# Kernel optimization log

Measured on AMD Instinct MI355X. Metric: run time of the kernel, lower is better.

Reference implementation:

```python
import jax, jax.numpy as jnp
import numpy as np


def setup_inputs() -> dict:
    key = jax.random.key(0)
    ks = jax.random.split(key, 12)
    B, N, M, C = 2, 20000, 4096, 6
    S, K, J = 2, 25, 64          # scales, grid cells (2*2+1)^2, neighbors per cell
    Cin = C + 2                   # xy coords concatenated to features
    Cout = 64
    xyz = jax.random.normal(ks[0], (B, N, 3), dtype=jnp.float32)
    feature = jax.random.normal(ks[1], (B, N, C), dtype=jnp.float32)
    new_xyz = jax.random.normal(ks[2], (B, M, 3), dtype=jnp.float32)
    idx = jax.random.randint(ks[3], (S, B, M, K, J), 0, N, dtype=jnp.int32)
    weight = jax.random.uniform(ks[4], (S, B, M, K, J), dtype=jnp.float32)
    conv_w = jax.random.normal(ks[5], (Cout, Cin, K), dtype=jnp.float32) * 0.05
    conv_b = jnp.zeros((Cout,), dtype=jnp.float32)
    mlp_w0 = jax.random.normal(ks[6], (128, S * Cout), dtype=jnp.float32) * 0.05
    mlp_b0 = jnp.zeros((128,), dtype=jnp.float32)
    mlp_w1 = jax.random.normal(ks[7], (256, 128), dtype=jnp.float32) * 0.05
    mlp_b1 = jnp.zeros((256,), dtype=jnp.float32)
    return {"xyz": xyz, "feature": feature, "new_xyz": new_xyz, "idx": idx,
            "weight": weight, "conv_w": conv_w, "conv_b": conv_b,
            "mlp_w0": mlp_w0, "mlp_b0": mlp_b0, "mlp_w1": mlp_w1, "mlp_b1": mlp_b1}


def reference(xyz, feature, new_xyz, idx, weight, conv_w, conv_b,
              mlp_w0, mlp_b0, mlp_w1, mlp_b1):
    # xyz_feature = cat(xy, feature): (B, N, Cin)
    xf = jnp.concatenate([xyz[:, :, :2], feature], axis=-1)
    center2 = new_xyz[:, :, :2]  # (B, M, 2); remaining channels of center are zero

    def per_scale(idx_s, w_s):
        # idx_s, w_s: (B, M, K, J). Gather neighbor features then bilinear-weight.
        gathered = jax.vmap(lambda f, i: f[i])(xf, idx_s)     # (B, M, K, J, Cin)
        nf = jnp.einsum('bmkj,bmkjc->bmkc', w_s, gathered)    # (B, M, K, Cin)
        nf = nf.at[..., :2].add(-center2[:, :, None, :])      # subtract center (xy only)
        # conv2d with kernel (1, K) over the neighbor axis + ReLU
        out = jnp.einsum('bmkc,ock->bom', nf, conv_w) + conv_b[None, :, None]
        return jax.nn.relu(out)                                # (B, Cout, M)

    outs = [per_scale(idx[s], weight[s]) for s in range(idx.shape[0])]
    x = jnp.concatenate(outs, axis=1)                          # (B, S*Cout, M)
    # SharedMLP: 1x1 convs with ReLU (bn=False)
    x = jax.nn.relu(jnp.einsum('bcm,oc->bom', x, mlp_w0) + mlp_b0[None, :, None])
    x = jax.nn.relu(jnp.einsum('bcm,oc->bom', x, mlp_w1) + mlp_b1[None, :, None])
    result_feature = jnp.transpose(x, (0, 2, 1))               # (B, M, 256)
    return new_xyz, result_feature
```

## Files before the change

### kernel.cpp

```cpp
#include <hip/hip_runtime.h>

#define B 2
#define N 20000
#define M 4096
#define S 2
#define K 25
#define J 64
#define CIN 8
#define KJ (K*J)
#define TC 32
#define XP 36

__global__ __launch_bounds__(256) void prep_kernel(
    const float* __restrict__ xyz, const float* __restrict__ feature,
    const float* __restrict__ new_xyz, const float* __restrict__ conv_w,
    const float* __restrict__ w0, const float* __restrict__ w1,
    float* __restrict__ xf, float* __restrict__ conv_wT,
    float* __restrict__ w0T, float* __restrict__ w1T,
    float* __restrict__ out_newxyz) {
    const int T1 = B * N * CIN;
    const int T2 = 208 * 64;
    const int T3 = B * M * 3;
    const int T4 = 128 * 128;
    const int T5 = 128 * 256;
    int e = blockIdx.x * blockDim.x + threadIdx.x;
    if (e < T1) {
        int r = e >> 3, t = e & 7;
        xf[e] = (t < 2) ? xyz[r * 3 + t] : feature[r * 6 + (t - 2)];
    } else if (e < T1 + T2) {
        int e2 = e - T1;
        int i = e2 >> 6, o = e2 & 63;
        conv_wT[e2] = (i < 200) ? conv_w[o * 200 + (i & 7) * 25 + (i >> 3)] : 0.f;
    } else if (e < T1 + T2 + T3) {
        int e3 = e - T1 - T2;
        out_newxyz[e3] = new_xyz[e3];
    } else if (e < T1 + T2 + T3 + T4) {
        int e4 = e - T1 - T2 - T3;
        int c = e4 >> 7, o = e4 & 127;
        w0T[e4] = w0[o * 128 + c];
    } else if (e < T1 + T2 + T3 + T4 + T5) {
        int e5 = e - T1 - T2 - T3 - T4;
        int c = e5 >> 8, o = e5 & 255;
        w1T[e5] = w1[o * 128 + c];
    }
}

__global__ __launch_bounds__(256) void gather_conv_kernel(
    const int* __restrict__ idx, const float* __restrict__ weight,
    const float* __restrict__ new_xyz, const float* __restrict__ xf,
    const float* __restrict__ conv_wT, const float* __restrict__ conv_b,
    float* __restrict__ xmid) {
    __shared__ float snf[208];
    __shared__ float spart[4][64];

    int g = blockIdx.x;
    int m = g & (M - 1);
    int sb = g >> 12;
    int b = sb & (B - 1);
    int s = sb >> 1;
    int tid = threadIdx.x;

    if (tid >= 200 && tid < 208) snf[tid] = 0.f;

    if (tid < 200) {
        int k = tid >> 3, jg = tid & 7;
        (void)k;
        const int4*   gi4 = (const int4*)  (idx    + (size_t)g * KJ);
        const float4* gw4 = (const float4*)(weight + (size_t)g * KJ);
        int4   ia = gi4[tid * 2], ib = gi4[tid * 2 + 1];
        float4 wa = gw4[tid * 2], wb = gw4[tid * 2 + 1];

        const float4* xfb = (const float4*)(xf + (size_t)b * N * CIN);
        float acc[8] = {0.f,0.f,0.f,0.f,0.f,0.f,0.f,0.f};
        int   rows[8] = {ia.x, ia.y, ia.z, ia.w, ib.x, ib.y, ib.z, ib.w};
        float wsv[8]  = {wa.x, wa.y, wa.z, wa.w, wb.x, wb.y, wb.z, wb.w};
        #pragma unroll
        for (int j = 0; j < 8; ++j) {
            float4 lo = xfb[rows[j] * 2];
            float4 hi = xfb[rows[j] * 2 + 1];
            float w = wsv[j];
            acc[0] = fmaf(w, lo.x, acc[0]);
            acc[1] = fmaf(w, lo.y, acc[1]);
            acc[2] = fmaf(w, lo.z, acc[2]);
            acc[3] = fmaf(w, lo.w, acc[3]);
            acc[4] = fmaf(w, hi.x, acc[4]);
            acc[5] = fmaf(w, hi.y, acc[5]);
            acc[6] = fmaf(w, hi.z, acc[6]);
            acc[7] = fmaf(w, hi.w, acc[7]);
        }
        #pragma unroll
        for (int d = 1; d < 8; d <<= 1) {
            #pragma unroll
            for (int c = 0; c < 8; ++c) acc[c] += __shfl_xor(acc[c], d, 64);
        }
        if (jg == 0) {
            int kk = tid >> 3;
            float cx = new_xyz[(b * M + m) * 3 + 0];
            float cy = new_xyz[(b * M + m) * 3 + 1];
            acc[0] -= cx; acc[1] -= cy;
            float4* s4 = (float4*)&snf[kk * 8];
            s4[0] = make_float4(acc[0], acc[1], acc[2], acc[3]);
            s4[1] = make_float4(acc[4], acc[5], acc[6], acc[7]);
        }
    }
    __syncthreads();

    int o = tid & 63, p = tid >> 6;
    const float4* snf4 = (const float4*)snf;
    float acc2 = 0.f;
    #pragma unroll
    for (int q = 0; q < 13; ++q) {
        float4 v = snf4[p * 13 + q];
        int i = (p * 13 + q) * 4;
        acc2 = fmaf(v.x, conv_wT[(i + 0) * 64 + o], acc2);
        acc2 = fmaf(v.y, conv_wT[(i + 1) * 64 + o], acc2);
        acc2 = fmaf(v.z, conv_wT[(i + 2) * 64 + o], acc2);
        acc2 = fmaf(v.w, conv_wT[(i + 3) * 64 + o], acc2);
    }
    spart[p][o] = acc2;
    __syncthreads();

    if (tid < 64) {
        float v = spart[0][tid] + spart[1][tid] + spart[2][tid] + spart[3][tid] + conv_b[tid];
        v = fmaxf(v, 0.f);
        xmid[((size_t)(b * M + m)) * 128 + s * 64 + tid] = v;
    }
}

__global__ __launch_bounds__(256) void mlp_kernel(
    const float* __restrict__ xmid,
    const float* __restrict__ w0T, const float* __restrict__ b0,
    const float* __restrict__ w1T, const float* __restrict__ b1,
    float* __restrict__ out_rf) {
    __shared__ float xs[128 * XP];
    __shared__ float ys0[128 * XP];

    int tid = threadIdx.x;
    int col0 = blockIdx.x * TC;

    {
        const float4* xm4 = (const float4*)(xmid + (size_t)col0 * 128);
        #pragma unroll
        for (int r = tid; r < 32 * TC; r += 256) {
            int lc = r >> 5, c4 = r & 31;
            float4 v = xm4[lc * 32 + c4];
            int c = c4 * 4;
            xs[(c + 0) * XP + lc] = v.x;
            xs[(c + 1) * XP + lc] = v.y;
            xs[(c + 2) * XP + lc] = v.z;
            xs[(c + 3) * XP + lc] = v.w;
        }
    }
    __syncthreads();

    {
        int og = tid >> 3, cg = tid & 7;
        int o0 = og * 4, lc0 = cg * 4;
        float acc[4][4];
        #pragma unroll
        for (int i = 0; i < 4; ++i) {
            float bv = b0[o0 + i];
            #pragma unroll
            for (int u = 0; u < 4; ++u) acc[i][u] = bv;
        }
        for (int c = 0; c < 128; ++c) {
            float4 xv = *(const float4*)&xs[c * XP + lc0];
            float4 wv = *(const float4*)&w0T[c * 128 + o0];
            acc[0][0] = fmaf(wv.x, xv.x, acc[0][0]);
            acc[0][1] = fmaf(wv.x, xv.y, acc[0][1]);
            acc[0][2] = fmaf(wv.x, xv.z, acc[0][2]);
            acc[0][3] = fmaf(wv.x, xv.w, acc[0][3]);
            acc[1][0] = fmaf(wv.y, xv.x, acc[1][0]);
            acc[1][1] = fmaf(wv.y, xv.y, acc[1][1]);
            acc[1][2] = fmaf(wv.y, xv.z, acc[1][2]);
            acc[1][3] = fmaf(wv.y, xv.w, acc[1][3]);
            acc[2][0] = fmaf(wv.z, xv.x, acc[2][0]);
            acc[2][1] = fmaf(wv.z, xv.y, acc[2][1]);
            acc[2][2] = fmaf(wv.z, xv.z, acc[2][2]);
            acc[2][3] = fmaf(wv.z, xv.w, acc[2][3]);
            acc[3][0] = fmaf(wv.w, xv.x, acc[3][0]);
            acc[3][1] = fmaf(wv.w, xv.y, acc[3][1]);
            acc[3][2] = fmaf(wv.w, xv.z, acc[3][2]);
            acc[3][3] = fmaf(wv.w, xv.w, acc[3][3]);
        }
        #pragma unroll
        for (int i = 0; i < 4; ++i)
            #pragma unroll
            for (int u = 0; u < 4; ++u)
                ys0[(o0 + i) * XP + lc0 + u] = fmaxf(acc[i][u], 0.f);
    }
    __syncthreads();

    {
        int og = tid >> 2, cg = tid & 3;
        int o0 = og * 4, lc0 = cg * 8;
        float acc[4][8];
        #pragma unroll
        for (int i = 0; i < 4; ++i) {
            float bv = b1[o0 + i];
            #pragma unroll
            for (int u = 0; u < 8; ++u) acc[i][u] = bv;
        }
        for (int c = 0; c < 128; ++c) {
            float4 xa = *(const float4*)&ys0[c * XP + lc0];
            float4 xb = *(const float4*)&ys0[c * XP + lc0 + 4];
            float4 wv = *(const float4*)&w1T[c * 256 + o0];
            float xv[8] = {xa.x, xa.y, xa.z, xa.w, xb.x, xb.y, xb.z, xb.w};
            #pragma unroll
            for (int i = 0; i < 4; ++i) {
                float w = (i == 0) ? wv.x : (i == 1) ? wv.y : (i == 2) ? wv.z : wv.w;
                #pragma unroll
                for (int u = 0; u < 8; ++u)
                    acc[i][u] = fmaf(w, xv[u], acc[i][u]);
            }
        }
        #pragma unroll
        for (int u = 0; u < 8; ++u) {
            float4 v = make_float4(fmaxf(acc[0][u], 0.f), fmaxf(acc[1][u], 0.f),
                                   fmaxf(acc[2][u], 0.f), fmaxf(acc[3][u], 0.f));
            *(float4*)&out_rf[(size_t)(col0 + lc0 + u) * 256 + o0] = v;
        }
    }
}

extern "C" void kernel_launch(void* const* d_in, const int* in_sizes, int n_in,
                              void* d_out, int out_size, void* d_ws, size_t ws_size,
                              hipStream_t stream) {
    const float* xyz     = (const float*)d_in[0];
    const float* feature = (const float*)d_in[1];
    const float* new_xyz = (const float*)d_in[2];
    const int*   idx     = (const int*)  d_in[3];
    const float* weight  = (const float*)d_in[4];
    const float* conv_w  = (const float*)d_in[5];
    const float* conv_b  = (const float*)d_in[6];
    const float* mlp_w0  = (const float*)d_in[7];
    const float* mlp_b0  = (const float*)d_in[8];
    const float* mlp_w1  = (const float*)d_in[9];
    const float* mlp_b1  = (const float*)d_in[10];

    float* out    = (float*)d_out;
    float* out_rf = out + (size_t)B * M * 3;

    float* xf      = (float*)d_ws;
    float* conv_wT = xf + 320000;
    float* xmid    = conv_wT + 13312;
    float* w0T     = xmid + 1048576;
    float* w1T     = w0T + 16384;

    {
        int total = 320000 + 13312 + 24576 + 16384 + 32768;
        int blocks = (total + 255) / 256;
        prep_kernel<<<blocks, 256, 0, stream>>>(xyz, feature, new_xyz, conv_w,
                                                mlp_w0, mlp_w1,
                                                xf, conv_wT, w0T, w1T, out);
    }
    {
        int blocks = S * B * M;
        gather_conv_kernel<<<blocks, 256, 0, stream>>>(idx, weight, new_xyz, xf,
                                                       conv_wT, conv_b, xmid);
    }
    {
        int blocks = (B * M) / TC;
        mlp_kernel<<<blocks, 256, 0, stream>>>(xmid, w0T, mlp_b0, w1T, mlp_b1,
                                               out_rf);
    }
}
```

Baseline: 387.3 us.

## Store gathered point features in bf16 and split MLP into two LDS-weighted kernels

```diff
diff --git a/kernel.cpp b/kernel.cpp
--- a/kernel.cpp
+++ b/kernel.cpp
@@ -1,4 +1,5 @@
 #include <hip/hip_runtime.h>
+#include <hip/hip_bf16.h>
 
 #define B 2
 #define N 20000
@@ -6,19 +7,20 @@
 #define S 2
 #define K 25
 #define J 64
-#define CIN 8
 #define KJ (K*J)
 #define TC 32
 #define XP 36
+
+typedef unsigned int u32;
 
 __global__ __launch_bounds__(256) void prep_kernel(
     const float* __restrict__ xyz, const float* __restrict__ feature,
     const float* __restrict__ new_xyz, const float* __restrict__ conv_w,
     const float* __restrict__ w0, const float* __restrict__ w1,
-    float* __restrict__ xf, float* __restrict__ conv_wT,
+    __hip_bfloat16* __restrict__ xfh, float* __restrict__ conv_wT,
     float* __restrict__ w0T, float* __restrict__ w1T,
     float* __restrict__ out_newxyz) {
-    const int T1 = B * N * CIN;
+    const int T1 = B * N * 8;
     const int T2 = 208 * 64;
     const int T3 = B * M * 3;
     const int T4 = 128 * 128;
@@ -26,7 +28,8 @@
     int e = blockIdx.x * blockDim.x + threadIdx.x;
     if (e < T1) {
         int r = e >> 3, t = e & 7;
-        xf[e] = (t < 2) ? xyz[r * 3 + t] : feature[r * 6 + (t - 2)];
+        float v = (t < 2) ? xyz[r * 3 + t] : feature[r * 6 + (t - 2)];
+        xfh[e] = __float2bfloat16(v);
     } else if (e < T1 + T2) {
         int e2 = e - T1;
         int i = e2 >> 6, o = e2 & 63;
@@ -47,7 +50,7 @@
 
 __global__ __launch_bounds__(256) void gather_conv_kernel(
     const int* __restrict__ idx, const float* __restrict__ weight,
-    const float* __restrict__ new_xyz, const float* __restrict__ xf,
+    const float* __restrict__ new_xyz, const uint4* __restrict__ xfh,
     const float* __restrict__ conv_wT, const float* __restrict__ conv_b,
     float* __restrict__ xmid) {
     __shared__ float snf[208];
@@ -63,37 +66,34 @@
     if (tid >= 200 && tid < 208) snf[tid] = 0.f;
 
     if (tid < 200) {
-        int k = tid >> 3, jg = tid & 7;
-        (void)k;
         const int4*   gi4 = (const int4*)  (idx    + (size_t)g * KJ);
         const float4* gw4 = (const float4*)(weight + (size_t)g * KJ);
         int4   ia = gi4[tid * 2], ib = gi4[tid * 2 + 1];
         float4 wa = gw4[tid * 2], wb = gw4[tid * 2 + 1];
 
-        const float4* xfb = (const float4*)(xf + (size_t)b * N * CIN);
+        const uint4* xfb = xfh + (size_t)b * N;
         float acc[8] = {0.f,0.f,0.f,0.f,0.f,0.f,0.f,0.f};
         int   rows[8] = {ia.x, ia.y, ia.z, ia.w, ib.x, ib.y, ib.z, ib.w};
         float wsv[8]  = {wa.x, wa.y, wa.z, wa.w, wb.x, wb.y, wb.z, wb.w};
         #pragma unroll
         for (int j = 0; j < 8; ++j) {
-            float4 lo = xfb[rows[j] * 2];
-            float4 hi = xfb[rows[j] * 2 + 1];
+            uint4 r = xfb[rows[j]];
             float w = wsv[j];
-            acc[0] = fmaf(w, lo.x, acc[0]);
-            acc[1] = fmaf(w, lo.y, acc[1]);
-            acc[2] = fmaf(w, lo.z, acc[2]);
-            acc[3] = fmaf(w, lo.w, acc[3]);
-            acc[4] = fmaf(w, hi.x, acc[4]);
-            acc[5] = fmaf(w, hi.y, acc[5]);
-            acc[6] = fmaf(w, hi.z, acc[6]);
-            acc[7] = fmaf(w, hi.w, acc[7]);
+            acc[0] = fmaf(w, __uint_as_float(r.x << 16),          acc[0]);
+            acc[1] = fmaf(w, __uint_as_float(r.x & 0xffff0000u),  acc[1]);
+            acc[2] = fmaf(w, __uint_as_float(r.y << 16),          acc[2]);
+            acc[3] = fmaf(w, __uint_as_float(r.y & 0xffff0000u),  acc[3]);
+            acc[4] = fmaf(w, __uint_as_float(r.z << 16),          acc[4]);
+            acc[5] = fmaf(w, __uint_as_float(r.z & 0xffff0000u),  acc[5]);
+            acc[6] = fmaf(w, __uint_as_float(r.w << 16),          acc[6]);
+            acc[7] = fmaf(w, __uint_as_float(r.w & 0xffff0000u),  acc[7]);
         }
         #pragma unroll
         for (int d = 1; d < 8; d <<= 1) {
             #pragma unroll
             for (int c = 0; c < 8; ++c) acc[c] += __shfl_xor(acc[c], d, 64);
         }
-        if (jg == 0) {
+        if ((tid & 7) == 0) {
             int kk = tid >> 3;
             float cx = new_xyz[(b * M + m) * 3 + 0];
             float cy = new_xyz[(b * M + m) * 3 + 1];
@@ -127,17 +127,21 @@
     }
 }
 
-__global__ __launch_bounds__(256) void mlp_kernel(
-    const float* __restrict__ xmid,
-    const float* __restrict__ w0T, const float* __restrict__ b0,
-    const float* __restrict__ w1T, const float* __restrict__ b1,
-    float* __restrict__ out_rf) {
+__global__ __launch_bounds__(256) void mlp0_kernel(
+    float* __restrict__ xmid,
+    const float* __restrict__ w0T, const float* __restrict__ b0) {
+    __shared__ float ws[128 * 128];
     __shared__ float xs[128 * XP];
-    __shared__ float ys0[128 * XP];
 
     int tid = threadIdx.x;
     int col0 = blockIdx.x * TC;
 
+    {
+        const float4* w4 = (const float4*)w0T;
+        float4* ws4 = (float4*)ws;
+        #pragma unroll
+        for (int i = 0; i < 16; ++i) ws4[tid + 256 * i] = w4[tid + 256 * i];
+    }
     {
         const float4* xm4 = (const float4*)(xmid + (size_t)col0 * 128);
         #pragma unroll
@@ -153,73 +157,101 @@
     }
     __syncthreads();
 
-    {
-        int og = tid >> 3, cg = tid & 7;
-        int o0 = og * 4, lc0 = cg * 4;
-        float acc[4][4];
-        #pragma unroll
-        for (int i = 0; i < 4; ++i) {
-            float bv = b0[o0 + i];
-            #pragma unroll
-            for (int u = 0; u < 4; ++u) acc[i][u] = bv;
-        }
-        for (int c = 0; c < 128; ++c) {
-            float4 xv = *(const float4*)&xs[c * XP + lc0];
-            float4 wv = *(const float4*)&w0T[c * 128 + o0];
-            acc[0][0] = fmaf(wv.x, xv.x, acc[0][0]);
-            acc[0][1] = fmaf(wv.x, xv.y, acc[0][1]);
-            acc[0][2] = fmaf(wv.x, xv.z, acc[0][2]);
-            acc[0][3] = fmaf(wv.x, xv.w, acc[0][3]);
-            acc[1][0] = fmaf(wv.y, xv.x, acc[1][0]);
-            acc[1][1] = fmaf(wv.y, xv.y, acc[1][1]);
-            acc[1][2] = fmaf(wv.y, xv.z, acc[1][2]);
-            acc[1][3] = fmaf(wv.y, xv.w, acc[1][3]);
-            acc[2][0] = fmaf(wv.z, xv.x, acc[2][0]);
-            acc[2][1] = fmaf(wv.z, xv.y, acc[2][1]);
-            acc[2][2] = fmaf(wv.z, xv.z, acc[2][2]);
-            acc[2][3] = fmaf(wv.z, xv.w, acc[2][3]);
-            acc[3][0] = fmaf(wv.w, xv.x, acc[3][0]);
-            acc[3][1] = fmaf(wv.w, xv.y, acc[3][1]);
-            acc[3][2] = fmaf(wv.w, xv.z, acc[3][2]);
-            acc[3][3] = fmaf(wv.w, xv.w, acc[3][3]);
-        }
-        #pragma unroll
-        for (int i = 0; i < 4; ++i)
-            #pragma unroll
-            for (int u = 0; u < 4; ++u)
-                ys0[(o0 + i) * XP + lc0 + u] = fmaxf(acc[i][u], 0.f);
+    int og = tid >> 3, cg = tid & 7;
+    int o0 = og * 4, lc0 = cg * 4;
+    float acc[4][4];
+    #pragma unroll
+    for (int i = 0; i < 4; ++i) {
+        float bv = b0[o0 + i];
+        #pragma unroll
+        for (int u = 0; u < 4; ++u) acc[i][u] = bv;
+    }
+    for (int c = 0; c < 128; ++c) {
+        float4 xv = *(const float4*)&xs[c * XP + lc0];
+        float4 wv = *(const float4*)&ws[c * 128 + o0];
+        acc[0][0] = fmaf(wv.x, xv.x, acc[0][0]);
+        acc[0][1] = fmaf(wv.x, xv.y, acc[0][1]);
+        acc[0][2] = fmaf(wv.x, xv.z, acc[0][2]);
+        acc[0][3] = fmaf(wv.x, xv.w, acc[0][3]);
+        acc[1][0] = fmaf(wv.y, xv.x, acc[1][0]);
+        acc[1][1] = fmaf(wv.y, xv.y, acc[1][1]);
+        acc[1][2] = fmaf(wv.y, xv.z, acc[1][2]);
+        acc[1][3] = fmaf(wv.y, xv.w, acc[1][3]);
+        acc[2][0] = fmaf(wv.z, xv.x, acc[2][0]);
+        acc[2][1] = fmaf(wv.z, xv.y, acc[2][1]);
+        acc[2][2] = fmaf(wv.z, xv.z, acc[2][2]);
+        acc[2][3] = fmaf(wv.z, xv.w, acc[2][3]);
+        acc[3][0] = fmaf(wv.w, xv.x, acc[3][0]);
+        acc[3][1] = fmaf(wv.w, xv.y, acc[3][1]);
+        acc[3][2] = fmaf(wv.w, xv.z, acc[3][2]);
+        acc[3][3] = fmaf(wv.w, xv.w, acc[3][3]);
+    }
+    #pragma unroll
+    for (int u = 0; u < 4; ++u) {
+        float4 v = make_float4(fmaxf(acc[0][u], 0.f), fmaxf(acc[1][u], 0.f),
+                               fmaxf(acc[2][u], 0.f), fmaxf(acc[3][u], 0.f));
+        *(float4*)&xmid[(size_t)(col0 + lc0 + u) * 128 + o0] = v;
+    }
+}
+
+__global__ __launch_bounds__(256) void mlp1_kernel(
+    const float* __restrict__ xmid,
+    const float* __restrict__ w1T, const float* __restrict__ b1,
+    float* __restrict__ out_rf) {
+    __shared__ float ws[128 * 256];
+    __shared__ float xs[128 * XP];
+
+    int tid = threadIdx.x;
+    int col0 = blockIdx.x * TC;
+
+    {
+        const float4* w4 = (const float4*)w1T;
+        float4* ws4 = (float4*)ws;
+        #pragma unroll
+        for (int i = 0; i < 32; ++i) ws4[tid + 256 * i] = w4[tid + 256 * i];
+    }
+    {
+        const float4* xm4 = (const float4*)(xmid + (size_t)col0 * 128);
+        #pragma unroll
+        for (int r = tid; r < 32 * TC; r += 256) {
+            int lc = r >> 5, c4 = r & 31;
+            float4 v = xm4[lc * 32 + c4];
+            int c = c4 * 4;
+            xs[(c + 0) * XP + lc] = v.x;
+            xs[(c + 1) * XP + lc] = v.y;
+            xs[(c + 2) * XP + lc] = v.z;
+            xs[(c + 3) * XP + lc] = v.w;
+        }
     }
     __syncthreads();
 
-    {
-        int og = tid >> 2, cg = tid & 3;
-        int o0 = og * 4, lc0 = cg * 8;
-        float acc[4][8];
-        #pragma unroll
-        for (int i = 0; i < 4; ++i) {
-            float bv = b1[o0 + i];
-            #pragma unroll
-            for (int u = 0; u < 8; ++u) acc[i][u] = bv;
-        }
-        for (int c = 0; c < 128; ++c) {
-            float4 xa = *(const float4*)&ys0[c * XP + lc0];
-            float4 xb = *(const float4*)&ys0[c * XP + lc0 + 4];
-            float4 wv = *(const float4*)&w1T[c * 256 + o0];
-            float xv[8] = {xa.x, xa.y, xa.z, xa.w, xb.x, xb.y, xb.z, xb.w};
-            #pragma unroll
-            for (int i = 0; i < 4; ++i) {
-                float w = (i == 0) ? wv.x : (i == 1) ? wv.y : (i == 2) ? wv.z : wv.w;
-                #pragma unroll
-                for (int u = 0; u < 8; ++u)
-                    acc[i][u] = fmaf(w, xv[u], acc[i][u]);
-            }
-        }
+    int og = tid >> 2, cg = tid & 3;
+    int o0 = og * 4, lc0 = cg * 8;
+    float acc[4][8];
+    #pragma unroll
+    for (int i = 0; i < 4; ++i) {
+        float bv = b1[o0 + i];
+        #pragma unroll
+        for (int u = 0; u < 8; ++u) acc[i][u] = bv;
+    }
+    for (int c = 0; c < 128; ++c) {
+        float4 xa = *(const float4*)&xs[c * XP + lc0];
+        float4 xb = *(const float4*)&xs[c * XP + lc0 + 4];
+        float4 wv = *(const float4*)&ws[c * 256 + o0];
+        float xv[8] = {xa.x, xa.y, xa.z, xa.w, xb.x, xb.y, xb.z, xb.w};
         #pragma unroll
         for (int u = 0; u < 8; ++u) {
-            float4 v = make_float4(fmaxf(acc[0][u], 0.f), fmaxf(acc[1][u], 0.f),
-                                   fmaxf(acc[2][u], 0.f), fmaxf(acc[3][u], 0.f));
-            *(float4*)&out_rf[(size_t)(col0 + lc0 + u) * 256 + o0] = v;
-        }
+            acc[0][u] = fmaf(wv.x, xv[u], acc[0][u]);
+            acc[1][u] = fmaf(wv.y, xv[u], acc[1][u]);
+            acc[2][u] = fmaf(wv.z, xv[u], acc[2][u]);
+            acc[3][u] = fmaf(wv.w, xv[u], acc[3][u]);
+        }
+    }
+    #pragma unroll
+    for (int u = 0; u < 8; ++u) {
+        float4 v = make_float4(fmaxf(acc[0][u], 0.f), fmaxf(acc[1][u], 0.f),
+                               fmaxf(acc[2][u], 0.f), fmaxf(acc[3][u], 0.f));
+        *(float4*)&out_rf[(size_t)(col0 + lc0 + u) * 256 + o0] = v;
     }
 }
 
@@ -241,8 +273,9 @@
     float* out    = (float*)d_out;
     float* out_rf = out + (size_t)B * M * 3;
 
-    float* xf      = (float*)d_ws;
-    float* conv_wT = xf + 320000;
+    float* wsf = (float*)d_ws;
+    __hip_bfloat16* xfh = (__hip_bfloat16*)wsf;
+    float* conv_wT = wsf + 160000;
     float* xmid    = conv_wT + 13312;
     float* w0T     = xmid + 1048576;
     float* w1T     = w0T + 16384;
@@ -252,16 +285,20 @@
         int blocks = (total + 255) / 256;
         prep_kernel<<<blocks, 256, 0, stream>>>(xyz, feature, new_xyz, conv_w,
                                                 mlp_w0, mlp_w1,
-                                                xf, conv_wT, w0T, w1T, out);
+                                                xfh, conv_wT, w0T, w1T, out);
     }
     {
         int blocks = S * B * M;
-        gather_conv_kernel<<<blocks, 256, 0, stream>>>(idx, weight, new_xyz, xf,
+        gather_conv_kernel<<<blocks, 256, 0, stream>>>(idx, weight, new_xyz,
+                                                       (const uint4*)xfh,
                                                        conv_wT, conv_b, xmid);
     }
     {
         int blocks = (B * M) / TC;
-        mlp_kernel<<<blocks, 256, 0, stream>>>(xmid, w0T, mlp_b0, w1T, mlp_b1,
-                                               out_rf);
-    }
-}
+        mlp0_kernel<<<blocks, 256, 0, stream>>>(xmid, w0T, mlp_b0);
+    }
+    {
+        int blocks = (B * M) / TC;
+        mlp1_kernel<<<blocks, 256, 0, stream>>>(xmid, w1T, mlp_b1, out_rf);
+    }
+}
```

Measured after the change: 384.6 us. No clear change (-0.7%).
